# Optimization experiments

Hardware: AMD Instinct MI355X
Metric: run time of the kernel (lower is better)

## Reference

```python
import jax, jax.numpy as jnp
import numpy as np

B, S, C = 64, 256, 512
H, O, L = 1024, 1024, 4


def setup_inputs() -> dict:
    key = jax.random.key(0)
    ks = jax.random.split(key, 8)
    inp = {
        "x": jax.random.normal(ks[0], (B, S, C), dtype=jnp.float32),
        "hid_layer": jax.random.normal(ks[1], (B, L, H), dtype=jnp.float32),
        "fc1_w": jax.random.normal(ks[2], (H, H + C), dtype=jnp.float32) * (1.0 / np.sqrt(H + C)),
        "fc1_b": jax.random.normal(ks[3], (H,), dtype=jnp.float32) * 0.01,
        "fc2_w": jax.random.normal(ks[4], (O, H), dtype=jnp.float32) * (1.0 / np.sqrt(H)),
        "fc2_b": jax.random.normal(ks[5], (O,), dtype=jnp.float32) * 0.01,
        "lin_w": jax.random.normal(ks[6], (L - 1, H, H), dtype=jnp.float32) * (1.0 / np.sqrt(H)),
        "lin_b": jax.random.normal(ks[7], (L - 1, H), dtype=jnp.float32) * 0.01,
    }
    return inp


def reference(x, hid_layer, fc1_w, fc1_b, fc2_w, fc2_b, lin_w, lin_b):
    # x: [B,S,C] -> [S,B,C]; hid_layer: [B,L,H] -> [L,B,H]
    xs = jnp.transpose(x, (1, 0, 2))
    h = jnp.transpose(hid_layer, (1, 0, 2))
    h0 = h[0]          # layer-0 hidden: never updated in original code (constant)
    h_rest = h[1:]     # [L-1, B, H], evolves by repeated affine map
    n_inner = lin_w.shape[0]

    def step(carry, x_i):
        hr = carry  # [L-1, B, H]
        # hid_layer[i+1, j+1] = linears[j](hid_layer[i, j+1])
        h_new = jnp.einsum("lbh,lgh->lbg", hr, lin_w) + lin_b[:, None, :]
        xc = jnp.concatenate([x_i, h0], axis=1)            # [B, C+H]
        temp = jnp.tanh(xc @ fc1_w.T + fc1_b)              # [B, H]
        for j in range(n_inner):                           # static small loop
            temp = jnp.tanh(h_new[j] + temp)
        out = jax.nn.softmax(jax.nn.relu(temp @ fc2_w.T + fc2_b), axis=-1)
        return h_new, out

    _, outs = jax.lax.scan(step, h_rest, xs)
    return outs  # [S, B, O]
```

## Files before the change

kernel.cpp:

```cpp
#include <hip/hip_runtime.h>
#include <hip/hip_bf16.h>

#define Bn 64
#define Sn 256
#define Cn 512
#define Hn 1024
#define On 1024
#define NL 3

__global__ __launch_bounds__(256) void prep_kernel(const float* __restrict__ hid,
                                                   float* __restrict__ h0T) {
    __shared__ float T[64][65];
    int l = blockIdx.x >> 4;
    int kb = (blockIdx.x & 15) * 64;
    int tid = threadIdx.x;
    for (int e = tid; e < 1024; e += 256) {
        int b = e >> 4, k4 = (e & 15) * 4;
        float4 v = *(const float4*)&hid[(size_t)b * 4096 + (size_t)(l + 1) * 1024 + kb + k4];
        T[b][k4] = v.x; T[b][k4 + 1] = v.y; T[b][k4 + 2] = v.z; T[b][k4 + 3] = v.w;
    }
    __syncthreads();
    for (int e = tid; e < 1024; e += 256) {
        int k = e >> 4, b4 = (e & 15) * 4;
        float4 v = make_float4(T[b4][k], T[b4 + 1][k], T[b4 + 2][k], T[b4 + 3][k]);
        *(float4*)&h0T[(size_t)l * 65536 + (size_t)(kb + k) * 64 + b4] = v;
    }
}

__global__ __launch_bounds__(256) void g1_kernel(const float* __restrict__ hid,
                                                 const float* __restrict__ fc1_w,
                                                 const float* __restrict__ fc1_b,
                                                 float* __restrict__ h0proj) {
    __shared__ __align__(16) float h0s[Hn];
    int b = blockIdx.x;
    int tid = threadIdx.x;
    for (int i = tid; i < Hn; i += 256) h0s[i] = hid[(size_t)b * 4 * Hn + i];
    __syncthreads();
    for (int g = tid; g < Hn; g += 256) {
        const float* wr = fc1_w + (size_t)g * (Cn + Hn) + Cn;
        float acc = 0.f;
        for (int k = 0; k < Hn; k += 4) {
            float4 w4 = *(const float4*)&wr[k];
            acc = fmaf(w4.x, h0s[k + 0], acc);
            acc = fmaf(w4.y, h0s[k + 1], acc);
            acc = fmaf(w4.z, h0s[k + 2], acc);
            acc = fmaf(w4.w, h0s[k + 3], acc);
        }
        h0proj[b * Hn + g] = acc + fc1_b[g];
    }
}

__global__ __launch_bounds__(256) void g2_kernel(const float* __restrict__ x,
                                                 const float* __restrict__ fc1_w,
                                                 const float* __restrict__ h0proj,
                                                 __hip_bfloat16* __restrict__ tb) {
    __shared__ __align__(16) float As[64][64];
    __shared__ __align__(16) float Bs[64][64];
    int tid = threadIdx.x;
    int bx = blockIdx.x;
    int g0 = blockIdx.y * 64;
    int ml = tid & 63;
    int kq = tid >> 6;
    const float* xrow = x + (size_t)ml * (Sn * Cn) + (size_t)bx * Cn;
    const float* wrow = fc1_w + (size_t)(g0 + ml) * (Cn + Hn);
    int wave = tid >> 6, lane = tid & 63;
    int tm = (wave & 1) * 32 + (lane & 7) * 4;
    int tg = (wave >> 1) * 32 + (lane >> 3) * 4;
    float acc[4][4] = {};
    for (int kc = 0; kc < Cn / 64; ++kc) {
#pragma unroll
        for (int r = 0; r < 4; ++r) {
            int kk = kq * 16 + r * 4;
            float4 v = *(const float4*)&xrow[kc * 64 + kk];
            As[kk + 0][ml] = v.x; As[kk + 1][ml] = v.y;
            As[kk + 2][ml] = v.z; As[kk + 3][ml] = v.w;
        }
#pragma unroll
        for (int r = 0; r < 4; ++r) {
            int kk = kq * 16 + r * 4;
            float4 v = *(const float4*)&wrow[kc * 64 + kk];
            Bs[kk + 0][ml] = v.x; Bs[kk + 1][ml] = v.y;
            Bs[kk + 2][ml] = v.z; Bs[kk + 3][ml] = v.w;
        }
        __syncthreads();
#pragma unroll 4
        for (int k = 0; k < 64; ++k) {
            float4 a4 = *(const float4*)&As[k][tm];
            float4 b4 = *(const float4*)&Bs[k][tg];
            float av[4] = {a4.x, a4.y, a4.z, a4.w};
            float bv[4] = {b4.x, b4.y, b4.z, b4.w};
#pragma unroll
            for (int i = 0; i < 4; ++i)
#pragma unroll
                for (int j = 0; j < 4; ++j)
                    acc[i][j] = fmaf(av[i], bv[j], acc[i][j]);
        }
        __syncthreads();
    }
#pragma unroll
    for (int j = 0; j < 4; ++j) {
        int g = g0 + tg + j;
        union { ushort4 u4; __hip_bfloat16 h[4]; } cv;
#pragma unroll
        for (int i = 0; i < 4; ++i) {
            float hp = h0proj[(size_t)(tm + i) * Hn + g];
            cv.h[i] = __float2bfloat16(tanhf(acc[i][j] + hp));
        }
        *(ushort4*)&tb[((size_t)bx * Hn + g) * 64 + tm] = cv.u4;
    }
}

__global__ __launch_bounds__(256) void g3_kernel(const __hip_bfloat16* __restrict__ tb,
                                                 const float* __restrict__ fc2_w,
                                                 const float* __restrict__ fc2_b,
                                                 float* __restrict__ logits) {
    __shared__ __align__(16) float As[64][64];
    __shared__ __align__(16) float Bs[64][64];
    int tid = threadIdx.x;
    int bx = blockIdx.x;
    int g0 = blockIdx.y * 64;
    int ml = tid & 63;
    int kq = tid >> 6;
    const float* wrow = fc2_w + (size_t)(g0 + ml) * Hn;
    int wave = tid >> 6, lane = tid & 63;
    int tm = (wave & 1) * 32 + (lane & 7) * 4;
    int tg = (wave >> 1) * 32 + (lane >> 3) * 4;
    float acc[4][4] = {};
    for (int kc = 0; kc < Hn / 64; ++kc) {
        for (int e = tid; e < 4096; e += 256) {
            int kk = e >> 6, mm = e & 63;
            As[kk][mm] = __bfloat162float(tb[((size_t)bx * Hn + kc * 64 + kk) * 64 + mm]);
        }
#pragma unroll
        for (int r = 0; r < 4; ++r) {
            int kk = kq * 16 + r * 4;
            float4 v = *(const float4*)&wrow[kc * 64 + kk];
            Bs[kk + 0][ml] = v.x; Bs[kk + 1][ml] = v.y;
            Bs[kk + 2][ml] = v.z; Bs[kk + 3][ml] = v.w;
        }
        __syncthreads();
#pragma unroll 4
        for (int k = 0; k < 64; ++k) {
            float4 a4 = *(const float4*)&As[k][tm];
            float4 b4 = *(const float4*)&Bs[k][tg];
            float av[4] = {a4.x, a4.y, a4.z, a4.w};
            float bv[4] = {b4.x, b4.y, b4.z, b4.w};
#pragma unroll
            for (int i = 0; i < 4; ++i)
#pragma unroll
                for (int j = 0; j < 4; ++j)
                    acc[i][j] = fmaf(av[i], bv[j], acc[i][j]);
        }
        __syncthreads();
    }
    int m0 = bx * 64;
#pragma unroll
    for (int i = 0; i < 4; ++i) {
        int m = m0 + tm + i;
        float4 o;
        o.x = fmaxf(acc[i][0] + fc2_b[g0 + tg + 0], 0.f);
        o.y = fmaxf(acc[i][1] + fc2_b[g0 + tg + 1], 0.f);
        o.z = fmaxf(acc[i][2] + fc2_b[g0 + tg + 2], 0.f);
        o.w = fmaxf(acc[i][3] + fc2_b[g0 + tg + 3], 0.f);
        *(float4*)&logits[(size_t)m * Hn + g0 + tg] = o;
    }
}

__global__ __launch_bounds__(256) void cvec_kernel(const float* __restrict__ A,
                                                   const float* __restrict__ vecB,
                                                   const float* __restrict__ addB,
                                                   float* __restrict__ outv) {
    int row = blockIdx.x * 4 + (threadIdx.x >> 6);
    int lane = threadIdx.x & 63;
    int l = row >> 10;
    const float* ar = A + (size_t)row * Hn;
    const float* vb = vecB + (size_t)l * Hn;
    float s = 0.f;
#pragma unroll 4
    for (int j = 0; j < 16; ++j) {
        int k = lane + j * 64;
        s = fmaf(ar[k], vb[k], s);
    }
    s += __shfl_xor(s, 1);  s += __shfl_xor(s, 2);  s += __shfl_xor(s, 4);
    s += __shfl_xor(s, 8);  s += __shfl_xor(s, 16); s += __shfl_xor(s, 32);
    if (lane == 0) outv[row] = s + addB[row];
}

__global__ __launch_bounds__(512, 2) void gsl_kernel(
        const float* __restrict__ A,
        const float* __restrict__ Bsrc,
        unsigned long long bPanel, int bstride, int bcol0, int ncols,
        float* __restrict__ dst, int dstride, int dcol0,
        const float* __restrict__ addRow,
        __hip_bfloat16* __restrict__ tb, const float* __restrict__ Xf,
        int folds, int do_gemm) {
    __shared__ __align__(16) float Bsh[2][16][256];
    const int tid = threadIdx.x;
    const int wg  = blockIdx.x;
    const int g0  = wg * 16;
    const int l   = g0 >> 10;

    if (folds >= 0) {
        for (int e = wg * 512 + tid; e < 4 * Hn * Bn; e += 192 * 512) {
            int b = e & 63, g = (e >> 6) & 1023, tp = e >> 16;
            int c = tp * 64 + b;
            size_t tix = ((size_t)(4 * folds + tp) * Hn + g) * 64 + b;
            float tv = __bfloat162float(tb[tix]);
            tv = tanhf(Xf[(size_t)g * 256 + c] + tv);
            tv = tanhf(Xf[(size_t)262144 + (size_t)g * 256 + c] + tv);
            tv = tanhf(Xf[(size_t)524288 + (size_t)g * 256 + c] + tv);
            tb[tix] = __float2bfloat16(tv);
        }
    }
    if (!do_gemm) return;

    const int cq = tid & 127;
    const int rq = tid >> 7;
    const int rbase = __builtin_amdgcn_readfirstlane(g0 + 4 * rq);
    const float* Ar0 = A + (size_t)rbase * Hn;
    const float* Ar1 = Ar0 + Hn;
    const float* Ar2 = Ar0 + 2 * Hn;
    const float* Ar3 = Ar0 + 3 * Hn;
    const float* Bp = Bsrc + (size_t)l * bPanel + bcol0;

    int sk, sc;
    bool sact;
    if (ncols == 256) { sk = tid >> 5; sc = (tid & 31) * 8; sact = true; }
    else              { sk = tid >> 3; sc = (tid & 7) * 8;  sact = (tid < 128); }
    const bool cact = (2 * cq < ncols);

    float acc[4][2] = {};
    float4 p0, p1;

    if (sact) {
        const float* src = Bp + (size_t)sk * bstride + sc;
        p0 = *(const float4*)(src);
        p1 = *(const float4*)(src + 4);
        *(float4*)&Bsh[0][sk][sc] = p0;
        *(float4*)&Bsh[0][sk][sc + 4] = p1;
    }
    __syncthreads();

    for (int ck = 0; ck < 64; ++ck) {
        if (ck < 63 && sact) {
            const float* src = Bp + (size_t)((ck + 1) * 16 + sk) * bstride + sc;
            p0 = *(const float4*)(src);
            p1 = *(const float4*)(src + 4);
        }
        if (cact) {
            const int k0 = ck * 16;
            const float* bs = &Bsh[ck & 1][0][2 * cq];
#pragma unroll
            for (int kk = 0; kk < 16; ++kk) {
                float w0 = Ar0[k0 + kk];
                float w1 = Ar1[k0 + kk];
                float w2 = Ar2[k0 + kk];
                float w3 = Ar3[k0 + kk];
                float2 b2 = *(const float2*)(bs + kk * 256);
                acc[0][0] = fmaf(w0, b2.x, acc[0][0]);
                acc[0][1] = fmaf(w0, b2.y, acc[0][1]);
                acc[1][0] = fmaf(w1, b2.x, acc[1][0]);
                acc[1][1] = fmaf(w1, b2.y, acc[1][1]);
                acc[2][0] = fmaf(w2, b2.x, acc[2][0]);
                acc[2][1] = fmaf(w2, b2.y, acc[2][1]);
                acc[3][0] = fmaf(w3, b2.x, acc[3][0]);
                acc[3][1] = fmaf(w3, b2.y, acc[3][1]);
            }
        }
        if (ck < 63) {
            if (sact) {
                *(float4*)&Bsh[(ck + 1) & 1][sk][sc] = p0;
                *(float4*)&Bsh[(ck + 1) & 1][sk][sc + 4] = p1;
            }
            __syncthreads();
        }
    }

    if (cact) {
#pragma unroll
        for (int i = 0; i < 4; ++i) {
            float av = addRow ? addRow[rbase + i] : 0.0f;
            float* d = dst + (size_t)(rbase + i) * dstride + dcol0 + 2 * cq;
            d[0] = acc[i][0] + av;
            d[1] = acc[i][1] + av;
        }
    }
}

__global__ __launch_bounds__(256) void softmax_kernel(const float* __restrict__ logits,
                                                      float* __restrict__ out) {
    __shared__ float redm[4];
    __shared__ float reds[4];
    __shared__ float bcast[2];
    int row = blockIdx.x, tid = threadIdx.x;
    const float* in = logits + (size_t)row * On;
    float4 v = *(const float4*)&in[tid * 4];
    float mx = fmaxf(fmaxf(v.x, v.y), fmaxf(v.z, v.w));
#pragma unroll
    for (int o = 32; o > 0; o >>= 1) mx = fmaxf(mx, __shfl_down(mx, o));
    if ((tid & 63) == 0) redm[tid >> 6] = mx;
    __syncthreads();
    if (tid == 0) bcast[0] = fmaxf(fmaxf(redm[0], redm[1]), fmaxf(redm[2], redm[3]));
    __syncthreads();
    float M = bcast[0];
    float e0 = expf(v.x - M), e1 = expf(v.y - M), e2 = expf(v.z - M), e3 = expf(v.w - M);
    float s = e0 + e1 + e2 + e3;
#pragma unroll
    for (int o = 32; o > 0; o >>= 1) s += __shfl_down(s, o);
    if ((tid & 63) == 0) reds[tid >> 6] = s;
    __syncthreads();
    if (tid == 0) bcast[1] = reds[0] + reds[1] + reds[2] + reds[3];
    __syncthreads();
    float inv = 1.0f / bcast[1];
    float4 o4 = make_float4(e0 * inv, e1 * inv, e2 * inv, e3 * inv);
    *(float4*)&out[(size_t)row * On + tid * 4] = o4;
}

extern "C" void kernel_launch(void* const* d_in, const int* in_sizes, int n_in,
                              void* d_out, int out_size, void* d_ws, size_t ws_size,
                              hipStream_t stream) {
    const float* x     = (const float*)d_in[0];
    const float* hid   = (const float*)d_in[1];
    const float* fc1_w = (const float*)d_in[2];
    const float* fc1_b = (const float*)d_in[3];
    const float* fc2_w = (const float*)d_in[4];
    const float* fc2_b = (const float*)d_in[5];
    const float* lin_w = (const float*)d_in[6];
    const float* lin_b = (const float*)d_in[7];
    float* out = (float*)d_out;

    char* wsb = (char*)d_ws;
    __hip_bfloat16* tb = (__hip_bfloat16*)wsb;
    float* logits = (float*)(wsb + 33554432ull);
    float* w2     = (float*)(wsb + 100663296ull);
    float* w4     = (float*)(wsb + 113246208ull);
    float* X      = (float*)(wsb + 125829120ull);
    float* c2     = (float*)(wsb + 132120576ull);
    float* c4     = (float*)(wsb + 132132864ull);
    float* h0T    = (float*)(wsb + 132145152ull);
    float* h0proj = (float*)(wsb + 132931584ull);

    float* X0 = X;
    float* X1 = X + 786432;

    prep_kernel<<<48, 256, 0, stream>>>(hid, h0T);
    g1_kernel<<<Bn, 256, 0, stream>>>(hid, fc1_w, fc1_b, h0proj);
    g2_kernel<<<dim3(Sn, Hn / 64), 256, 0, stream>>>(x, fc1_w, h0proj, tb);

    cvec_kernel<<<768, 256, 0, stream>>>(lin_w, lin_b, lin_b, c2);
    for (int p = 0; p < 4; ++p)
        gsl_kernel<<<192, 512, 0, stream>>>(lin_w, lin_w, 1048576ull, 1024, p * 256, 256,
                                            w2, 1024, p * 256, nullptr,
                                            tb, nullptr, -1, 1);
    cvec_kernel<<<768, 256, 0, stream>>>(w2, c2, c2, c4);
    for (int p = 0; p < 4; ++p)
        gsl_kernel<<<192, 512, 0, stream>>>(w2, w2, 1048576ull, 1024, p * 256, 256,
                                            w4, 1024, p * 256, nullptr,
                                            tb, nullptr, -1, 1);
    gsl_kernel<<<192, 512, 0, stream>>>(lin_w, h0T, 65536ull, 64, 0, 64,
                                        X0, 256, 0, lin_b, tb, nullptr, -1, 1);
    gsl_kernel<<<192, 512, 0, stream>>>(w2, h0T, 65536ull, 64, 0, 64,
                                        X0, 256, 64, c2, tb, nullptr, -1, 1);
    gsl_kernel<<<192, 512, 0, stream>>>(w4, h0T, 65536ull, 64, 0, 64,
                                        X0, 256, 192, c4, tb, nullptr, -1, 1);
    gsl_kernel<<<192, 512, 0, stream>>>(w2, X0, 262144ull, 256, 0, 64,
                                        X0, 256, 128, c2, tb, nullptr, -1, 1);

    for (int s = 0; s < 63; ++s) {
        float* Xin  = (s & 1) ? X1 : X0;
        float* Xout = (s & 1) ? X0 : X1;
        gsl_kernel<<<192, 512, 0, stream>>>(w4, Xin, 262144ull, 256, 0, 256,
                                            Xout, 256, 0, c4, tb, Xin, s, 1);
    }
    gsl_kernel<<<192, 512, 0, stream>>>(w4, X1, 262144ull, 256, 0, 256,
                                        X0, 256, 0, c4, tb, X1, 63, 0);

    g3_kernel<<<dim3(Sn, Hn / 64), 256, 0, stream>>>(tb, fc2_w, fc2_b, logits);
    softmax_kernel<<<Sn * Bn, 256, 0, stream>>>(logits, out);
}
```

Measured before the change: 5.109 ms.

## Advance recurrence eight steps per launch using precomputed W^8 panel

Squares the inner affine map once more to form W^8 and its offset c8. The sequential scan now advances eight timesteps per launch instead of four, which halves the number of dependent launches, and each launch handles 512 columns. The GEMM kernel is templated on column width, computes 8 rows per thread with float2 stores, and swizzles block indices across layers. The cost is an extra 3x1024^3 squaring GEMM, larger workspace buffers, and more accumulated floating-point error from the higher matrix power.

After: 8.049 ms. +57.5%, slower.

```diff
diff --git a/kernel.cpp b/kernel.cpp
--- a/kernel.cpp
+++ b/kernel.cpp
@@ -186,91 +186,101 @@
     if (lane == 0) outv[row] = s + addB[row];
 }
 
-__global__ __launch_bounds__(512, 2) void gsl_kernel(
+template<int NC>
+__global__ __launch_bounds__(512, 2) void gsl2_kernel(
         const float* __restrict__ A,
         const float* __restrict__ Bsrc,
-        unsigned long long bPanel, int bstride, int bcol0, int ncols,
+        unsigned long long bPanel, int bstride, int bcol0,
         float* __restrict__ dst, int dstride, int dcol0,
         const float* __restrict__ addRow,
         __hip_bfloat16* __restrict__ tb, const float* __restrict__ Xf,
         int folds, int do_gemm) {
-    __shared__ __align__(16) float Bsh[2][16][256];
+    __shared__ __align__(16) float Bsh[2][16][NC];
     const int tid = threadIdx.x;
-    const int wg  = blockIdx.x;
-    const int g0  = wg * 16;
-    const int l   = g0 >> 10;
+    const int bid = blockIdx.x;
+    const int lbid = (bid & 7) * 24 + (bid >> 3);
+    const int row0 = lbid * 16;
+    const int l = row0 >> 10;
 
     if (folds >= 0) {
-        for (int e = wg * 512 + tid; e < 4 * Hn * Bn; e += 192 * 512) {
+        for (int e = bid * 512 + tid; e < 8 * Hn * Bn; e += 192 * 512) {
             int b = e & 63, g = (e >> 6) & 1023, tp = e >> 16;
             int c = tp * 64 + b;
-            size_t tix = ((size_t)(4 * folds + tp) * Hn + g) * 64 + b;
+            size_t tix = ((size_t)(8 * folds + tp) * Hn + g) * 64 + b;
             float tv = __bfloat162float(tb[tix]);
-            tv = tanhf(Xf[(size_t)g * 256 + c] + tv);
-            tv = tanhf(Xf[(size_t)262144 + (size_t)g * 256 + c] + tv);
-            tv = tanhf(Xf[(size_t)524288 + (size_t)g * 256 + c] + tv);
+            tv = tanhf(Xf[(size_t)g * 512 + c] + tv);
+            tv = tanhf(Xf[524288 + (size_t)g * 512 + c] + tv);
+            tv = tanhf(Xf[1048576 + (size_t)g * 512 + c] + tv);
             tb[tix] = __float2bfloat16(tv);
         }
     }
     if (!do_gemm) return;
 
-    const int cq = tid & 127;
-    const int rq = tid >> 7;
-    const int rbase = __builtin_amdgcn_readfirstlane(g0 + 4 * rq);
-    const float* Ar0 = A + (size_t)rbase * Hn;
-    const float* Ar1 = Ar0 + Hn;
-    const float* Ar2 = Ar0 + 2 * Hn;
-    const float* Ar3 = Ar0 + 3 * Hn;
-    const float* Bp = Bsrc + (size_t)l * bPanel + bcol0;
-
-    int sk, sc;
-    bool sact;
-    if (ncols == 256) { sk = tid >> 5; sc = (tid & 31) * 8; sact = true; }
-    else              { sk = tid >> 3; sc = (tid & 7) * 8;  sact = (tid < 128); }
-    const bool cact = (2 * cq < ncols);
-
-    float acc[4][2] = {};
-    float4 p0, p1;
-
-    if (sact) {
-        const float* src = Bp + (size_t)sk * bstride + sc;
-        p0 = *(const float4*)(src);
-        p1 = *(const float4*)(src + 4);
-        *(float4*)&Bsh[0][sk][sc] = p0;
-        *(float4*)&Bsh[0][sk][sc + 4] = p1;
+    const int rq = tid >> 8;
+    const int cq = tid & 255;
+    const int rbase = __builtin_amdgcn_readfirstlane(row0 + rq * 8);
+    const float* __restrict__ A8 = A + (size_t)rbase * 1024;
+    const float* __restrict__ Bp = Bsrc + (size_t)l * bPanel + bcol0;
+    constexpr int NF4 = NC / 4;
+    constexpr int TOT4 = 16 * NF4;
+    constexpr int PFN = (TOT4 + 511) / 512;
+    const bool cact = (2 * cq < NC);
+
+    float acc[8][2] = {};
+    float4 pf[PFN];
+
+#pragma unroll
+    for (int i = 0; i < PFN; ++i) {
+        int e = tid + i * 512;
+        if ((TOT4 % 512 == 0) || e < TOT4) {
+            int k = e / NF4, c4 = e % NF4;
+            pf[i] = *(const float4*)(Bp + (size_t)k * bstride + c4 * 4);
+        }
+    }
+#pragma unroll
+    for (int i = 0; i < PFN; ++i) {
+        int e = tid + i * 512;
+        if ((TOT4 % 512 == 0) || e < TOT4) {
+            int k = e / NF4, c4 = e % NF4;
+            *(float4*)&Bsh[0][k][c4 * 4] = pf[i];
+        }
     }
     __syncthreads();
 
     for (int ck = 0; ck < 64; ++ck) {
-        if (ck < 63 && sact) {
-            const float* src = Bp + (size_t)((ck + 1) * 16 + sk) * bstride + sc;
-            p0 = *(const float4*)(src);
-            p1 = *(const float4*)(src + 4);
+        if (ck < 63) {
+#pragma unroll
+            for (int i = 0; i < PFN; ++i) {
+                int e = tid + i * 512;
+                if ((TOT4 % 512 == 0) || e < TOT4) {
+                    int k = e / NF4, c4 = e % NF4;
+                    pf[i] = *(const float4*)(Bp + (size_t)((ck + 1) * 16 + k) * bstride + c4 * 4);
+                }
+            }
         }
         if (cact) {
+            const float* bsc = &Bsh[ck & 1][0][2 * cq];
             const int k0 = ck * 16;
-            const float* bs = &Bsh[ck & 1][0][2 * cq];
 #pragma unroll
             for (int kk = 0; kk < 16; ++kk) {
-                float w0 = Ar0[k0 + kk];
-                float w1 = Ar1[k0 + kk];
-                float w2 = Ar2[k0 + kk];
-                float w3 = Ar3[k0 + kk];
-                float2 b2 = *(const float2*)(bs + kk * 256);
-                acc[0][0] = fmaf(w0, b2.x, acc[0][0]);
-                acc[0][1] = fmaf(w0, b2.y, acc[0][1]);
-                acc[1][0] = fmaf(w1, b2.x, acc[1][0]);
-                acc[1][1] = fmaf(w1, b2.y, acc[1][1]);
-                acc[2][0] = fmaf(w2, b2.x, acc[2][0]);
-                acc[2][1] = fmaf(w2, b2.y, acc[2][1]);
-                acc[3][0] = fmaf(w3, b2.x, acc[3][0]);
-                acc[3][1] = fmaf(w3, b2.y, acc[3][1]);
+                float2 b2 = *(const float2*)(bsc + kk * NC);
+                const float* Ap = A8 + k0 + kk;
+#pragma unroll
+                for (int i = 0; i < 8; ++i) {
+                    float av = Ap[(size_t)i * 1024];
+                    acc[i][0] = fmaf(av, b2.x, acc[i][0]);
+                    acc[i][1] = fmaf(av, b2.y, acc[i][1]);
+                }
             }
         }
         if (ck < 63) {
-            if (sact) {
-                *(float4*)&Bsh[(ck + 1) & 1][sk][sc] = p0;
-                *(float4*)&Bsh[(ck + 1) & 1][sk][sc + 4] = p1;
+#pragma unroll
+            for (int i = 0; i < PFN; ++i) {
+                int e = tid + i * 512;
+                if ((TOT4 % 512 == 0) || e < TOT4) {
+                    int k = e / NF4, c4 = e % NF4;
+                    *(float4*)&Bsh[(ck + 1) & 1][k][c4 * 4] = pf[i];
+                }
             }
             __syncthreads();
         }
@@ -278,11 +288,11 @@
 
     if (cact) {
 #pragma unroll
-        for (int i = 0; i < 4; ++i) {
-            float av = addRow ? addRow[rbase + i] : 0.0f;
-            float* d = dst + (size_t)(rbase + i) * dstride + dcol0 + 2 * cq;
-            d[0] = acc[i][0] + av;
-            d[1] = acc[i][1] + av;
+        for (int i = 0; i < 8; ++i) {
+            int r = rbase + i;
+            float av = addRow ? addRow[r] : 0.0f;
+            float2 o = make_float2(acc[i][0] + av, acc[i][1] + av);
+            *(float2*)(dst + (size_t)r * dstride + dcol0 + 2 * cq) = o;
         }
     }
 }
@@ -331,49 +341,57 @@
 
     char* wsb = (char*)d_ws;
     __hip_bfloat16* tb = (__hip_bfloat16*)wsb;
+    float* w2     = (float*)(wsb + 33554432ull);
+    float* w4     = (float*)(wsb + 46137344ull);
+    float* w8     = (float*)(wsb + 58720256ull);
+    float* X0     = (float*)(wsb + 71303168ull);
+    float* X1     = (float*)(wsb + 77594624ull);
+    float* c2     = (float*)(wsb + 83886080ull);
+    float* c4     = (float*)(wsb + 83898368ull);
+    float* c8     = (float*)(wsb + 83910656ull);
+    float* h0T    = (float*)(wsb + 83922944ull);
+    float* h0proj = (float*)(wsb + 84709376ull);
     float* logits = (float*)(wsb + 33554432ull);
-    float* w2     = (float*)(wsb + 100663296ull);
-    float* w4     = (float*)(wsb + 113246208ull);
-    float* X      = (float*)(wsb + 125829120ull);
-    float* c2     = (float*)(wsb + 132120576ull);
-    float* c4     = (float*)(wsb + 132132864ull);
-    float* h0T    = (float*)(wsb + 132145152ull);
-    float* h0proj = (float*)(wsb + 132931584ull);
-
-    float* X0 = X;
-    float* X1 = X + 786432;
 
     prep_kernel<<<48, 256, 0, stream>>>(hid, h0T);
     g1_kernel<<<Bn, 256, 0, stream>>>(hid, fc1_w, fc1_b, h0proj);
     g2_kernel<<<dim3(Sn, Hn / 64), 256, 0, stream>>>(x, fc1_w, h0proj, tb);
 
     cvec_kernel<<<768, 256, 0, stream>>>(lin_w, lin_b, lin_b, c2);
-    for (int p = 0; p < 4; ++p)
-        gsl_kernel<<<192, 512, 0, stream>>>(lin_w, lin_w, 1048576ull, 1024, p * 256, 256,
-                                            w2, 1024, p * 256, nullptr,
-                                            tb, nullptr, -1, 1);
+    for (int p = 0; p < 2; ++p)
+        gsl2_kernel<512><<<192, 512, 0, stream>>>(lin_w, lin_w, 1048576ull, 1024, p * 512,
+                                                  w2, 1024, p * 512, nullptr,
+                                                  tb, nullptr, -1, 1);
     cvec_kernel<<<768, 256, 0, stream>>>(w2, c2, c2, c4);
-    for (int p = 0; p < 4; ++p)
-        gsl_kernel<<<192, 512, 0, stream>>>(w2, w2, 1048576ull, 1024, p * 256, 256,
-                                            w4, 1024, p * 256, nullptr,
-                                            tb, nullptr, -1, 1);
-    gsl_kernel<<<192, 512, 0, stream>>>(lin_w, h0T, 65536ull, 64, 0, 64,
-                                        X0, 256, 0, lin_b, tb, nullptr, -1, 1);
-    gsl_kernel<<<192, 512, 0, stream>>>(w2, h0T, 65536ull, 64, 0, 64,
-                                        X0, 256, 64, c2, tb, nullptr, -1, 1);
-    gsl_kernel<<<192, 512, 0, stream>>>(w4, h0T, 65536ull, 64, 0, 64,
-                                        X0, 256, 192, c4, tb, nullptr, -1, 1);
-    gsl_kernel<<<192, 512, 0, stream>>>(w2, X0, 262144ull, 256, 0, 64,
-                                        X0, 256, 128, c2, tb, nullptr, -1, 1);
-
-    for (int s = 0; s < 63; ++s) {
+    for (int p = 0; p < 2; ++p)
+        gsl2_kernel<512><<<192, 512, 0, stream>>>(w2, w2, 1048576ull, 1024, p * 512,
+                                                  w4, 1024, p * 512, nullptr,
+                                                  tb, nullptr, -1, 1);
+    cvec_kernel<<<768, 256, 0, stream>>>(w4, c4, c4, c8);
+    for (int p = 0; p < 2; ++p)
+        gsl2_kernel<512><<<192, 512, 0, stream>>>(w4, w4, 1048576ull, 1024, p * 512,
+                                                  w8, 1024, p * 512, nullptr,
+                                                  tb, nullptr, -1, 1);
+
+    gsl2_kernel<64><<<192, 512, 0, stream>>>(lin_w, h0T, 65536ull, 64, 0,
+                                             X0, 512, 0, lin_b, tb, nullptr, -1, 1);
+    gsl2_kernel<64><<<192, 512, 0, stream>>>(w2, h0T, 65536ull, 64, 0,
+                                             X0, 512, 64, c2, tb, nullptr, -1, 1);
+    gsl2_kernel<64><<<192, 512, 0, stream>>>(w4, h0T, 65536ull, 64, 0,
+                                             X0, 512, 192, c4, tb, nullptr, -1, 1);
+    gsl2_kernel<64><<<192, 512, 0, stream>>>(w2, X0, 524288ull, 512, 0,
+                                             X0, 512, 128, c2, tb, nullptr, -1, 1);
+    gsl2_kernel<256><<<192, 512, 0, stream>>>(w4, X0, 524288ull, 512, 0,
+                                              X0, 512, 256, c4, tb, nullptr, -1, 1);
+
+    for (int s = 0; s < 31; ++s) {
         float* Xin  = (s & 1) ? X1 : X0;
         float* Xout = (s & 1) ? X0 : X1;
-        gsl_kernel<<<192, 512, 0, stream>>>(w4, Xin, 262144ull, 256, 0, 256,
-                                            Xout, 256, 0, c4, tb, Xin, s, 1);
-    }
-    gsl_kernel<<<192, 512, 0, stream>>>(w4, X1, 262144ull, 256, 0, 256,
-                                        X0, 256, 0, c4, tb, X1, 63, 0);
+        gsl2_kernel<512><<<192, 512, 0, stream>>>(w8, Xin, 524288ull, 512, 0,
+                                                  Xout, 512, 0, c8, tb, Xin, s, 1);
+    }
+    gsl2_kernel<512><<<192, 512, 0, stream>>>(w8, X1, 524288ull, 512, 0,
+                                              X0, 512, 0, c8, tb, X1, 31, 0);
 
     g3_kernel<<<dim3(Sn, Hn / 64), 256, 0, stream>>>(tb, fc2_w, fc2_b, logits);
     softmax_kernel<<<Sn * Bn, 256, 0, stream>>>(logits, out);
```
